# Performance work log

Hardware: AMD Instinct MI355X
Metric: run time of the kernel (lower is better)

Reference implementation:

```python
import jax, jax.numpy as jnp
import numpy as np

DOMAIN_MIN, DOMAIN_MAX = -1.0, 1.0
N, D_IN, D_OUT, K = 1024, 128, 128, 8


def setup_inputs() -> dict:
    key = jax.random.key(0)
    k1, k2, k3 = jax.random.split(key, 3)
    x = jax.random.uniform(k1, (N, D_IN), dtype=jnp.float32,
                           minval=DOMAIN_MIN, maxval=DOMAIN_MAX)
    # Per-edge spline knot values: near-identity init plus small noise.
    base = jnp.linspace(DOMAIN_MIN, DOMAIN_MAX, K, dtype=jnp.float32)
    coeffs = base[None, None, :] + 0.1 * jax.random.normal(
        k2, (D_OUT, D_IN, K), dtype=jnp.float32)
    weights = jax.random.normal(k3, (D_OUT, D_IN), dtype=jnp.float32) * np.sqrt(2.0 / D_IN)
    bias = jnp.zeros((D_OUT,), dtype=jnp.float32)
    return {"x": x, "coeffs": coeffs, "weights": weights, "bias": bias}


def _spline_all_edges(x, coeffs):
    """Evaluate every edge's cubic (Catmull-Rom) spline at its input.
    x: [N, d_in]; coeffs: [d_out, d_in, K] knot values on uniform knots in [-1,1].
    Returns s: [N, d_in, d_out]."""
    K_ = coeffs.shape[-1]
    h = (DOMAIN_MAX - DOMAIN_MIN) / (K_ - 1)
    xc = jnp.clip(x, DOMAIN_MIN, DOMAIN_MAX)
    t = (xc - DOMAIN_MIN) / h                      # [N, d_in], in [0, K-1]
    idx = jnp.clip(jnp.floor(t).astype(jnp.int32), 0, K_ - 2)
    u = t - idx                                    # local coord in [0,1]
    i0 = jnp.clip(idx - 1, 0, K_ - 1)
    i1 = idx
    i2 = idx + 1
    i3 = jnp.clip(idx + 2, 0, K_ - 1)
    ct = jnp.transpose(coeffs, (1, 2, 0))          # [d_in, K, d_out]
    jar = jnp.arange(ct.shape[0])[None, :]          # [1, d_in]
    p0 = ct[jar, i0]                               # [N, d_in, d_out]
    p1 = ct[jar, i1]
    p2 = ct[jar, i2]
    p3 = ct[jar, i3]
    u2 = u * u
    u3 = u2 * u
    b0 = 0.5 * (-u3 + 2.0 * u2 - u)
    b1 = 0.5 * (3.0 * u3 - 5.0 * u2 + 2.0)
    b2 = 0.5 * (-3.0 * u3 + 4.0 * u2 + u)
    b3 = 0.5 * (u3 - u2)
    return (b0[..., None] * p0 + b1[..., None] * p1 +
            b2[..., None] * p2 + b3[..., None] * p3)


def reference(x, coeffs, weights, bias):
    # h_i(x) = sum_j w_ij * s_ij(x_j) + b_i
    s = _spline_all_edges(x, coeffs)               # [N, d_in, d_out]
    return jnp.einsum('njo,oj->no', s, weights) + bias[None, :]
```

## Files before the change

kernel.cpp:

```cpp
#include <hip/hip_runtime.h>
#include <hip/hip_bf16.h>
#include <stdint.h>


#define DIN 128
#define DOUT 128
#define KTOT 1024

typedef unsigned int u32;
typedef unsigned short u16;
typedef __attribute__((ext_vector_type(8))) short bf16x8;
typedef __attribute__((ext_vector_type(4))) float f32x4;

union H8 { u16 s[8]; uint4 v; };

__device__ __forceinline__ u16 f2b(float f) {
    union { __hip_bfloat16 h; u16 u; } c;
    c.h = __float2bfloat16(f);
    return c.u;
}

__global__ __launch_bounds__(1024) void kan_fused(
    const float* __restrict__ x, const float* __restrict__ coeffs,
    const float* __restrict__ weights, const float* __restrict__ bias,
    float* __restrict__ out)
{
    __shared__ __align__(16) u16 sBas[16 * KTOT];
    __shared__ __align__(16) u16 sWp [16 * KTOT];
    float* sC = (float*)sBas;

    const int tid  = threadIdx.x;
    const int wave = tid >> 6;
    const int lane = tid & 63;
    const int n0 = blockIdx.x * 16;
    const int o0 = blockIdx.y * 16;

    #pragma unroll
    for (int it = 0; it < 2; ++it) {
        const int task = tid + it * 1024;
        const int row = task >> 7;
        const int j = task & 127;
        float xv = x[n0 * DIN + task];
        xv = fminf(fmaxf(xv, -1.0f), 1.0f);
        const float t = (xv + 1.0f) * 3.5f;
        int idx = (int)t; idx = idx > 6 ? 6 : idx;
        const float u = t - (float)idx;
        const float u2 = u * u, u3 = u2 * u;
        const float b0 = 0.5f * (-u3 + 2.0f * u2 - u);
        const float b1 = 0.5f * (3.0f * u3 - 5.0f * u2 + 2.0f);
        const float b2 = 0.5f * (-3.0f * u3 + 4.0f * u2 + u);
        const float b3 = 0.5f * (u3 - u2);
        float r[8];
        #pragma unroll
        for (int k = 0; k < 8; ++k) r[k] = 0.0f;
        const int i0 = idx > 0 ? idx - 1 : 0;
        const int i3 = idx < 6 ? idx + 2 : 7;
        r[i0] += b0; r[idx] += b1; r[idx + 1] += b2; r[i3] += b3;
        H8 h;
        #pragma unroll
        for (int k = 0; k < 8; ++k) h.s[k] = f2b(r[k]);
        const int uu = j ^ (row & 7);
        *(uint4*)(sBas + row * KTOT + uu * 8) = h.v;
    }

    #pragma unroll
    for (int it = 0; it < 2; ++it) {
        const int task = tid + it * 1024;
        const int o = task >> 7;
        const int j = task & 127;
        const float wv = weights[o0 * DIN + task];
        const float4 c0 = *(const float4*)(coeffs + o0 * KTOT + task * 8);
        const float4 c1 = *(const float4*)(coeffs + o0 * KTOT + task * 8 + 4);
        H8 h;
        h.s[0] = f2b(c0.x * wv); h.s[1] = f2b(c0.y * wv);
        h.s[2] = f2b(c0.z * wv); h.s[3] = f2b(c0.w * wv);
        h.s[4] = f2b(c1.x * wv); h.s[5] = f2b(c1.y * wv);
        h.s[6] = f2b(c1.z * wv); h.s[7] = f2b(c1.w * wv);
        const int uu = j ^ (o & 7);
        *(uint4*)(sWp + o * KTOT + uu * 8) = h.v;
    }
    __syncthreads();

    const int mo = lane & 15;
    const int q  = lane >> 4;
    const int sw = mo & 7;
    f32x4 acc = {0.0f, 0.0f, 0.0f, 0.0f};
    #pragma unroll
    for (int s = 0; s < 2; ++s) {
        const int S = wave * 2 + s;
        const int uu = (S * 4 + q) ^ sw;
        bf16x8 af = *(const bf16x8*)(sBas + mo * KTOT + uu * 8);
        bf16x8 bf = *(const bf16x8*)(sWp  + mo * KTOT + uu * 8);
        acc = __builtin_amdgcn_mfma_f32_16x16x32_bf16(af, bf, acc, 0, 0, 0);
    }
    __syncthreads();

    #pragma unroll
    for (int r = 0; r < 4; ++r)
        sC[wave * 256 + (q * 4 + r) * 16 + mo] = acc[r];
    __syncthreads();

    if (tid < 256) {
        const int row = tid >> 4, col = tid & 15;
        float v = sC[tid];
        #pragma unroll
        for (int w = 1; w < 16; ++w) v += sC[w * 256 + tid];
        out[(n0 + row) * DOUT + o0 + col] = v + bias[o0 + col];
    }
}

extern "C" void kernel_launch(void* const* d_in, const int* in_sizes, int n_in,
                              void* d_out, int out_size, void* d_ws, size_t ws_size,
                              hipStream_t stream) {
    const float* x       = (const float*)d_in[0];
    const float* coeffs  = (const float*)d_in[1];
    const float* weights = (const float*)d_in[2];
    const float* bias    = (const float*)d_in[3];
    float* out = (float*)d_out;
    const int N = in_sizes[0] / DIN;
    dim3 grid(N / 16, DOUT / 16);
    kan_fused<<<grid, 1024, 0, stream>>>(x, coeffs, weights, bias, out);
}
```

Before: 62.66 us.

## Split into precompute kernel for basis/weighted coeffs and separate MFMA kernel

Before, every block recomputed the spline basis for its 16 rows and the weighted coefficients for its 16 outputs, so that work was repeated across the 8x64 grid. A new pre-kernel now computes each value once into bf16 workspace buffers. The matmul kernel then reads its MFMA operands straight from global memory instead of through shared memory. This costs an extra kernel launch and a global round-trip, and the operand loads are now uncoalesced 16-byte global reads.

```diff
diff --git a/kernel.cpp b/kernel.cpp
--- a/kernel.cpp
+++ b/kernel.cpp
@@ -20,31 +20,18 @@
     return c.u;
 }
 
-__global__ __launch_bounds__(1024) void kan_fused(
+__global__ __launch_bounds__(1024) void kan_pre(
     const float* __restrict__ x, const float* __restrict__ coeffs,
-    const float* __restrict__ weights, const float* __restrict__ bias,
-    float* __restrict__ out)
+    const float* __restrict__ weights, u16* __restrict__ gBas,
+    u16* __restrict__ gWp, int nBasis)
 {
-    __shared__ __align__(16) u16 sBas[16 * KTOT];
-    __shared__ __align__(16) u16 sWp [16 * KTOT];
-    float* sC = (float*)sBas;
-
-    const int tid  = threadIdx.x;
-    const int wave = tid >> 6;
-    const int lane = tid & 63;
-    const int n0 = blockIdx.x * 16;
-    const int o0 = blockIdx.y * 16;
-
-    #pragma unroll
-    for (int it = 0; it < 2; ++it) {
-        const int task = tid + it * 1024;
-        const int row = task >> 7;
-        const int j = task & 127;
-        float xv = x[n0 * DIN + task];
+    const int t = blockIdx.x * 1024 + threadIdx.x;
+    if (t < nBasis) {
+        float xv = x[t];
         xv = fminf(fmaxf(xv, -1.0f), 1.0f);
-        const float t = (xv + 1.0f) * 3.5f;
-        int idx = (int)t; idx = idx > 6 ? 6 : idx;
-        const float u = t - (float)idx;
+        const float tt = (xv + 1.0f) * 3.5f;
+        int idx = (int)tt; idx = idx > 6 ? 6 : idx;
+        const float u = tt - (float)idx;
         const float u2 = u * u, u3 = u2 * u;
         const float b0 = 0.5f * (-u3 + 2.0f * u2 - u);
         const float b1 = 0.5f * (3.0f * u3 - 5.0f * u2 + 2.0f);
@@ -59,41 +46,49 @@
         H8 h;
         #pragma unroll
         for (int k = 0; k < 8; ++k) h.s[k] = f2b(r[k]);
-        const int uu = j ^ (row & 7);
-        *(uint4*)(sBas + row * KTOT + uu * 8) = h.v;
+        *(uint4*)(gBas + (size_t)t * 8) = h.v;
+    } else {
+        const int u = t - nBasis;
+        if (u < DOUT * DIN) {
+            const float wv = weights[u];
+            const float4 c0 = *(const float4*)(coeffs + (size_t)u * 8);
+            const float4 c1 = *(const float4*)(coeffs + (size_t)u * 8 + 4);
+            H8 h;
+            h.s[0] = f2b(c0.x * wv); h.s[1] = f2b(c0.y * wv);
+            h.s[2] = f2b(c0.z * wv); h.s[3] = f2b(c0.w * wv);
+            h.s[4] = f2b(c1.x * wv); h.s[5] = f2b(c1.y * wv);
+            h.s[6] = f2b(c1.z * wv); h.s[7] = f2b(c1.w * wv);
+            *(uint4*)(gWp + (size_t)u * 8) = h.v;
+        }
     }
+}
 
-    #pragma unroll
-    for (int it = 0; it < 2; ++it) {
-        const int task = tid + it * 1024;
-        const int o = task >> 7;
-        const int j = task & 127;
-        const float wv = weights[o0 * DIN + task];
-        const float4 c0 = *(const float4*)(coeffs + o0 * KTOT + task * 8);
-        const float4 c1 = *(const float4*)(coeffs + o0 * KTOT + task * 8 + 4);
-        H8 h;
-        h.s[0] = f2b(c0.x * wv); h.s[1] = f2b(c0.y * wv);
-        h.s[2] = f2b(c0.z * wv); h.s[3] = f2b(c0.w * wv);
-        h.s[4] = f2b(c1.x * wv); h.s[5] = f2b(c1.y * wv);
-        h.s[6] = f2b(c1.z * wv); h.s[7] = f2b(c1.w * wv);
-        const int uu = j ^ (o & 7);
-        *(uint4*)(sWp + o * KTOT + uu * 8) = h.v;
-    }
-    __syncthreads();
+__global__ __launch_bounds__(1024) void kan_mm(
+    const u16* __restrict__ gBas, const u16* __restrict__ gWp,
+    const float* __restrict__ bias, float* __restrict__ out)
+{
+    __shared__ __align__(16) float sC[16 * 256];
+
+    const int tid  = threadIdx.x;
+    const int wave = tid >> 6;
+    const int lane = tid & 63;
+    const int n0 = blockIdx.x * 16;
+    const int o0 = blockIdx.y * 16;
 
     const int mo = lane & 15;
     const int q  = lane >> 4;
-    const int sw = mo & 7;
+    const u16* pA = gBas + (size_t)(n0 + mo) * KTOT;
+    const u16* pB = gWp  + (size_t)(o0 + mo) * KTOT;
+
     f32x4 acc = {0.0f, 0.0f, 0.0f, 0.0f};
     #pragma unroll
     for (int s = 0; s < 2; ++s) {
         const int S = wave * 2 + s;
-        const int uu = (S * 4 + q) ^ sw;
-        bf16x8 af = *(const bf16x8*)(sBas + mo * KTOT + uu * 8);
-        bf16x8 bf = *(const bf16x8*)(sWp  + mo * KTOT + uu * 8);
+        const int off = S * 32 + q * 8;
+        bf16x8 af = *(const bf16x8*)(pA + off);
+        bf16x8 bf = *(const bf16x8*)(pB + off);
         acc = __builtin_amdgcn_mfma_f32_16x16x32_bf16(af, bf, acc, 0, 0, 0);
     }
-    __syncthreads();
 
     #pragma unroll
     for (int r = 0; r < 4; ++r)
@@ -118,6 +113,15 @@
     const float* bias    = (const float*)d_in[3];
     float* out = (float*)d_out;
     const int N = in_sizes[0] / DIN;
+
+    u16* gBas = (u16*)d_ws;
+    u16* gWp  = gBas + (size_t)N * DIN * 8;
+    const int nBasis = N * DIN;
+    const int nTot   = nBasis + DOUT * DIN;
+
+    kan_pre<<<dim3((nTot + 1023) / 1024), 1024, 0, stream>>>(
+        x, coeffs, weights, gBas, gWp, nBasis);
+
     dim3 grid(N / 16, DOUT / 16);
-    kan_fused<<<grid, 1024, 0, stream>>>(x, coeffs, weights, bias, out);
+    kan_mm<<<grid, 1024, 0, stream>>>(gBas, gWp, bias, out);
 }
```

Measured after the change: 65.72 us. +4.9%, slower.
